# Kernel tuning notes

Hardware: AMD Instinct MI355X
Metric: run time of the kernel (lower is better)

The kernel has to match this reference:

```python
import jax, jax.numpy as jnp
import numpy as np

N_NODES = 100000
N_EDGES = 1600000
IN_DIM = 128
LATENT = [128, 128, 16]  # last entry = num classes (logits dim)


def setup_inputs() -> dict:
    key = jax.random.key(0)
    ks = jax.random.split(key, 16)
    inp = {
        "x": jax.random.normal(ks[0], (N_NODES, IN_DIM), dtype=jnp.float32),
        "edge_index": jax.random.randint(ks[1], (2, N_EDGES), 0, N_NODES, dtype=jnp.int64),
        "edge_weight": jax.random.uniform(ks[2], (N_EDGES,), dtype=jnp.float32),
    }
    dims = [IN_DIM] + LATENT
    for i in range(len(LATENT)):
        fan_in = dims[i]
        scale = 1.0 / np.sqrt(fan_in)
        inp[f"W{i}"] = jax.random.uniform(ks[3 + 2 * i], (dims[i], dims[i + 1]), minval=-scale, maxval=scale, dtype=jnp.float32)
        inp[f"b{i}"] = jax.random.uniform(ks[4 + 2 * i], (dims[i + 1],), minval=-scale, maxval=scale, dtype=jnp.float32)
        inp[f"eps{i}"] = jnp.zeros((), dtype=jnp.float32)  # GINConv train_eps init = 0
    return inp


def _gin_layer(x, W, b, eps, src, dst, edge_weight):
    # message: x_j (optionally scaled by edge weight), summed into target nodes
    msg = x[src]
    if edge_weight is not None:
        msg = msg * edge_weight[:, None]
    agg = jax.ops.segment_sum(msg, dst, num_segments=N_NODES)
    h = (1.0 + eps) * x + agg
    return jax.nn.relu(h @ W + b)  # MLP = Linear + ReLU


def _l2_normalize(x, eps=1e-12):
    norm = jnp.linalg.norm(x, axis=-1, keepdims=True)
    return x / jnp.maximum(norm, eps)


def reference(x, edge_index, edge_weight, W0, b0, eps0, W1, b1, eps1, W2, b2, eps2):
    src, dst = edge_index[0], edge_index[1]
    params = [(W0, b0, eps0), (W1, b1, eps1), (W2, b2, eps2)]
    h = x
    # all but last layer: GINConv(with edge_weight) -> l2 normalize -> ReLU
    for (W, b, e) in params[:-1]:
        h = _gin_layer(h, W, b, e, src, dst, edge_weight)
        h = _l2_normalize(h)  # emb_normlize=True
        h = jax.nn.relu(h)
    # last layer: GINConv WITHOUT edge_weight (forward passes only x, edge_index)
    W, b, e = params[-1]
    logits = _gin_layer(h, W, b, e, src, dst, None)
    probs = jax.nn.softmax(logits, axis=-1)
    return (logits, probs)
```

## Files before the change

kernel.cpp:

```cpp
#include <hip/hip_runtime.h>
#include <hip/hip_bf16.h>

#define N_NODES 100000
#define N_EDGES 1600000
#define DIM 128
#define ODIM 16
#define NB 391
#define PCHUNK 3200
#define PBLK 500
#define FCAP 4608
#define CB4 12500

typedef unsigned int uint32;
typedef float f32x2 __attribute__((ext_vector_type(2)));
typedef float f32x4 __attribute__((ext_vector_type(4)));
typedef short bf16x8 __attribute__((ext_vector_type(8)));
typedef uint32 u32x4 __attribute__((ext_vector_type(4)));
typedef uint32 u32x2 __attribute__((ext_vector_type(2)));

static __device__ __forceinline__ float bflo(uint32 p) { return __uint_as_float(p << 16); }
static __device__ __forceinline__ float bfhi(uint32 p) { return __uint_as_float(p & 0xFFFF0000u); }
static __device__ __forceinline__ unsigned short f2bf(float f) {
  __hip_bfloat16 h = __float2bfloat16(f);
  return *reinterpret_cast<unsigned short*>(&h);
}
static __device__ __forceinline__ uint32 pk2bf(float a, float b) {
  return (uint32)f2bf(a) | ((uint32)f2bf(b) << 16);
}

__global__ __launch_bounds__(256) void prep_kernel(
    const f32x4* __restrict__ x4, uint32* __restrict__ Xu,
    const float* __restrict__ W0, const float* __restrict__ W1,
    const float* __restrict__ W2,
    unsigned short* __restrict__ pW0, unsigned short* __restrict__ pW1,
    unsigned short* __restrict__ pW2,
    const int* __restrict__ dst, int* __restrict__ bcnt) {
  __shared__ int h[NB];
  int b = blockIdx.x;
  int tid = threadIdx.x;
  if (b < CB4) {
    int i = b * 256 + tid;
    f32x4 v = __builtin_nontemporal_load(x4 + i);
    u32x2 o = {pk2bf(v[0], v[1]), pk2bf(v[2], v[3])};
    *(u32x2*)(Xu + (size_t)i * 2) = o;
  } else if (b < CB4 + 128) {
    int wsel = (b - CB4) >> 6;
    int idx = ((b - CB4) & 63) * 256 + tid;
    int j = idx & 7, lane = (idx >> 3) & 63, nt = (idx >> 9) & 7, kc = idx >> 12;
    const float* W = wsel ? W1 : W0;
    unsigned short* pW = wsel ? pW1 : pW0;
    pW[idx] = f2bf(W[(kc * 32 + (lane >> 4) * 8 + j) * DIM + nt * 16 + (lane & 15)]);
  } else if (b < CB4 + 136) {
    int idx = (b - CB4 - 128) * 256 + tid;
    int j = idx & 7, lane = (idx >> 3) & 63, kc = idx >> 9;
    pW2[idx] = f2bf(W2[(kc * 32 + (lane >> 4) * 8 + j) * ODIM + (lane & 15)]);
  } else {
    for (int i = tid; i < NB; i += 256) h[i] = 0;
    __syncthreads();
    int e0 = (b - CB4 - 136) * PCHUNK;
    for (int i = tid; i < PCHUNK; i += 256)
      atomicAdd(&h[__builtin_nontemporal_load(dst + e0 + i) >> 8], 1);
    __syncthreads();
    for (int i = tid; i < NB; i += 256)
      if (h[i]) atomicAdd(&bcnt[i], h[i]);
  }
}

__global__ __launch_bounds__(256) void coarse_partition_kernel(
    const int* __restrict__ src, const int* __restrict__ dst,
    const float* __restrict__ ew, const int* __restrict__ bcnt,
    int* __restrict__ bcur, int2* __restrict__ epack) {
  __shared__ int hist[NB];
  __shared__ int base_a[NB];
  __shared__ int base_g[NB];
  __shared__ int lcur_a[NB];
  __shared__ int gbase_a[NB];
  __shared__ int2 stg[PCHUNK];
  __shared__ int gpos[PCHUNK];

  int tid = threadIdx.x;
  int e0 = blockIdx.x * PCHUNK;

  for (int i = tid; i < NB; i += 256) hist[i] = 0;
  __syncthreads();
  for (int i = tid; i < PCHUNK; i += 256) atomicAdd(&hist[dst[e0 + i] >> 8], 1);
  __syncthreads();

  if (tid < 64) {
    int run = 0, rung = 0;
#pragma unroll
    for (int c = 0; c < 7; c++) {
      int idx = c * 64 + tid;
      int v = (idx < NB) ? hist[idx] : 0;
      int vg = (idx < NB) ? bcnt[idx] : 0;
      int incl = v, inclg = vg;
#pragma unroll
      for (int off = 1; off < 64; off <<= 1) {
        int t1 = __shfl_up(incl, off, 64);
        int t2 = __shfl_up(inclg, off, 64);
        if (tid >= off) { incl += t1; inclg += t2; }
      }
      if (idx < NB) {
        base_a[idx] = run + incl - v;
        base_g[idx] = rung + inclg - vg;
      }
      run += __shfl(incl, 63, 64);
      rung += __shfl(inclg, 63, 64);
    }
  }
  __syncthreads();
  for (int i = tid; i < NB; i += 256) {
    int c = hist[i];
    gbase_a[i] = (c > 0) ? base_g[i] + atomicAdd(&bcur[i], c) : 0;
    lcur_a[i] = base_a[i];
  }
  __syncthreads();

  for (int i = tid; i < PCHUNK; i += 256) {
    int e = e0 + i;
    int s = __builtin_nontemporal_load(src + e);
    int d = dst[e];
    float w = __builtin_nontemporal_load(ew + e);
    int bkt = d >> 8;
    int pos = atomicAdd(&lcur_a[bkt], 1);
    stg[pos] = make_int2(s | ((d & 255) << 20), __float_as_int(w));
    gpos[pos] = gbase_a[bkt] + (pos - base_a[bkt]);
  }
  __syncthreads();
  for (int i = tid; i < PCHUNK; i += 256) epack[gpos[i]] = stg[i];
}

__global__ __launch_bounds__(256) void fine_sort_kernel(
    const int* __restrict__ bcnt, int2* __restrict__ epack,
    int* __restrict__ row_ptr) {
  __shared__ int2 ebuf[FCAP];
  __shared__ unsigned short inv[FCAP];
  __shared__ int hist[256];
  __shared__ int sc[256];
  __shared__ int cur[256];
  __shared__ int redc[4];
  int tid = threadIdx.x;
  int b = blockIdx.x;
  int node0 = b << 8;

  int part = 0;
  for (int i = tid; i < b; i += 256) part += bcnt[i];
#pragma unroll
  for (int off = 32; off >= 1; off >>= 1) part += __shfl_xor(part, off, 64);
  if ((tid & 63) == 0) redc[tid >> 6] = part;
  hist[tid] = 0;
  __syncthreads();
  int lo = redc[0] + redc[1] + redc[2] + redc[3];
  int n = bcnt[b];
  if (n > FCAP) n = FCAP;

  for (int i = tid; i < n; i += 256) {
    int2 e = epack[lo + i];
    ebuf[i] = e;
    atomicAdd(&hist[(e.x >> 20) & 255], 1);
  }
  __syncthreads();
  sc[tid] = hist[tid];
  __syncthreads();
  for (int off = 1; off < 256; off <<= 1) {
    int a2 = (tid >= off) ? sc[tid - off] : 0;
    __syncthreads();
    sc[tid] += a2;
    __syncthreads();
  }
  int excl = sc[tid] - hist[tid];
  if (node0 + tid < N_NODES) row_ptr[node0 + tid] = lo + excl;
  cur[tid] = excl;
  if (b == 0 && tid == 0) row_ptr[N_NODES] = N_EDGES;
  __syncthreads();
  for (int i = tid; i < n; i += 256) {
    int p = atomicAdd(&cur[(ebuf[i].x >> 20) & 255], 1);
    inv[p] = (unsigned short)i;
  }
  __syncthreads();
  for (int p = tid; p < n; p += 256) {
    int2 e = ebuf[inv[p]];
    epack[lo + p] = make_int2(e.x & 0xFFFFF, e.y);
  }
}

__global__ __launch_bounds__(256, 8) void gather_bf16(
    const uint32* __restrict__ hu, const int* __restrict__ row_ptr,
    const int2* __restrict__ ep, uint32* __restrict__ aggu) {
  int lane = threadIdx.x & 63;
  int node = blockIdx.x * 4 + (threadIdx.x >> 6);
  if (node >= N_NODES) return;
  int grp = lane >> 4, l4 = lane & 15;
  int a = row_ptr[node], bnd = row_ptr[node + 1];
  f32x2 acc2[4];
#pragma unroll
  for (int k = 0; k < 4; k++) acc2[k] = (f32x2){0.f, 0.f};

  auto acc8 = [&](float wv, const uint4& p) {
    acc2[0] += (f32x2){bflo(p.x), bfhi(p.x)} * wv;
    acc2[1] += (f32x2){bflo(p.y), bfhi(p.y)} * wv;
    acc2[2] += (f32x2){bflo(p.z), bfhi(p.z)} * wv;
    acc2[3] += (f32x2){bflo(p.w), bfhi(p.w)} * wv;
  };

#pragma unroll 2
  for (int j = a; j < bnd; j += 16) {
    int i0 = j + grp;
    int i1 = i0 + 4;
    int i2 = i0 + 8;
    int i3 = i0 + 12;
    int2 e0 = ep[i0 < bnd ? i0 : a];
    int2 e1 = ep[i1 < bnd ? i1 : a];
    int2 e2 = ep[i2 < bnd ? i2 : a];
    int2 e3 = ep[i3 < bnd ? i3 : a];
    uint4 p0 = *(const uint4*)(hu + (size_t)e0.x * 64 + l4 * 4);
    uint4 p1 = *(const uint4*)(hu + (size_t)e1.x * 64 + l4 * 4);
    uint4 p2 = *(const uint4*)(hu + (size_t)e2.x * 64 + l4 * 4);
    uint4 p3 = *(const uint4*)(hu + (size_t)e3.x * 64 + l4 * 4);
    float w0 = i0 < bnd ? __int_as_float(e0.y) : 0.f;
    float w1 = i1 < bnd ? __int_as_float(e1.y) : 0.f;
    float w2 = i2 < bnd ? __int_as_float(e2.y) : 0.f;
    float w3 = i3 < bnd ? __int_as_float(e3.y) : 0.f;
    acc8(w0, p0);
    acc8(w1, p1);
    acc8(w2, p2);
    acc8(w3, p3);
  }
#pragma unroll
  for (int k = 0; k < 4; k++) {
    acc2[k].x += __shfl_xor(acc2[k].x, 16, 64);
    acc2[k].x += __shfl_xor(acc2[k].x, 32, 64);
    acc2[k].y += __shfl_xor(acc2[k].y, 16, 64);
    acc2[k].y += __shfl_xor(acc2[k].y, 32, 64);
  }
  if (lane < 16) {
    u32x4 st = {pk2bf(acc2[0].x, acc2[0].y), pk2bf(acc2[1].x, acc2[1].y),
                pk2bf(acc2[2].x, acc2[2].y), pk2bf(acc2[3].x, acc2[3].y)};
    __builtin_nontemporal_store(st, (u32x4*)(aggu + (size_t)node * 64 + l4 * 4));
  }
}

template <int FUSE_PROJ>
__global__ __launch_bounds__(256) void gin_mlp_mfma(
    const uint32* Xu, const uint32* __restrict__ Au,
    const unsigned char* __restrict__ pW, const float* __restrict__ b,
    const float* __restrict__ eps_p, uint32* outH,
    const unsigned char* __restrict__ pW2, uint32* __restrict__ yb) {
  __shared__ __align__(16) unsigned char As[64 * 272];
  int tid = threadIdx.x;
  int node0 = blockIdx.x * 64;
  float epf = 1.0f + *eps_p;

  const uint4* X4 = (const uint4*)Xu;
  const uint4* A4 = (const uint4*)Au;
#pragma unroll
  for (int c = 0; c < 4; c++) {
    int t = c * 256 + tid;
    int n = t >> 4, s = t & 15;
    int node = node0 + n;
    int cn = node < N_NODES ? node : N_NODES - 1;
    uint4 xv = X4[(size_t)cn * 16 + s];
    uint4 av = A4[(size_t)cn * 16 + s];
    uint4 o;
    o.x = pk2bf(fmaf(epf, bflo(xv.x), bflo(av.x)), fmaf(epf, bfhi(xv.x), bfhi(av.x)));
    o.y = pk2bf(fmaf(epf, bflo(xv.y), bflo(av.y)), fmaf(epf, bfhi(xv.y), bfhi(av.y)));
    o.z = pk2bf(fmaf(epf, bflo(xv.z), bflo(av.z)), fmaf(epf, bfhi(xv.z), bfhi(av.z)));
    o.w = pk2bf(fmaf(epf, bflo(xv.w), bflo(av.w)), fmaf(epf, bfhi(xv.w), bfhi(av.w)));
    *(uint4*)(As + n * 272 + s * 16) = o;
  }
  __syncthreads();

  int w = tid >> 6, l = tid & 63;
  int m = l & 15, q = l >> 4;

  f32x4 acc[8];
#pragma unroll
  for (int nt = 0; nt < 8; nt++) acc[nt] = (f32x4){0.f, 0.f, 0.f, 0.f};

  const unsigned char* Abase = As + (w * 16 + m) * 272 + q * 16;
#pragma unroll
  for (int kc = 0; kc < 4; kc++) {
    bf16x8 af = *(const bf16x8*)(Abase + kc * 64);
#pragma unroll
    for (int nt = 0; nt < 8; nt++) {
      bf16x8 bfr = *(const bf16x8*)(pW + (size_t)((kc * 8 + nt) * 64 + l) * 16);
      acc[nt] = __builtin_amdgcn_mfma_f32_16x16x32_bf16(af, bfr, acc[nt], 0, 0, 0);
    }
  }

  float ss[4] = {0.f, 0.f, 0.f, 0.f};
#pragma unroll
  for (int nt = 0; nt < 8; nt++) {
    float bj = b[nt * 16 + m];
#pragma unroll
    for (int r = 0; r < 4; r++) {
      float v = fmaxf(acc[nt][r] + bj, 0.0f);
      acc[nt][r] = v;
      ss[r] += v * v;
    }
  }
#pragma unroll
  for (int r = 0; r < 4; r++) {
    float s = ss[r];
    s += __shfl_xor(s, 1, 64);
    s += __shfl_xor(s, 2, 64);
    s += __shfl_xor(s, 4, 64);
    s += __shfl_xor(s, 8, 64);
    ss[r] = 1.0f / fmaxf(sqrtf(s), 1e-12f);
  }
#pragma unroll
  for (int nt = 0; nt < 8; nt++) {
#pragma unroll
    for (int r = 0; r < 4; r++) {
      unsigned short hv = f2bf(acc[nt][r] * ss[r]);
      *(unsigned short*)(As + (w * 16 + q * 4 + r) * 272 + (nt * 16 + m) * 2) = hv;
    }
  }

  if (FUSE_PROJ) {
    f32x4 accy = (f32x4){0.f, 0.f, 0.f, 0.f};
#pragma unroll
    for (int kc = 0; kc < 4; kc++) {
      bf16x8 af = *(const bf16x8*)(Abase + kc * 64);
      bf16x8 bfr = *(const bf16x8*)(pW2 + (size_t)(kc * 64 + l) * 16);
      accy = __builtin_amdgcn_mfma_f32_16x16x32_bf16(af, bfr, accy, 0, 0, 0);
    }
#pragma unroll
    for (int r = 0; r < 4; r++) {
      float v = accy[r];
      float o = __shfl_xor(v, 1, 64);
      if (!(m & 1)) {
        int orow = node0 + w * 16 + q * 4 + r;
        if (orow < N_NODES) yb[(size_t)orow * 8 + (m >> 1)] = pk2bf(v, o);
      }
    }
  } else {
    __syncthreads();
    int rem = N_NODES - node0; if (rem > 64) rem = 64;
    for (int i = tid; i < 1024; i += 256) {
      int row = i >> 4, seg = i & 15;
      if (row < rem) {
        uint4 vv = *(const uint4*)(As + row * 272 + seg * 16);
        *(uint4*)((unsigned char*)outH + (size_t)(node0 + row) * 256 + seg * 16) = vv;
      }
    }
  }
}

__global__ __launch_bounds__(256) void gather16_final_kernel(
    const uint32* __restrict__ yb, const int* __restrict__ row_ptr,
    const int2* __restrict__ ep, const float* __restrict__ bb,
    const float* __restrict__ eps_p, float* __restrict__ out_logits,
    float* __restrict__ out_probs) {
  int lane = threadIdx.x & 63;
  int node = blockIdx.x * 4 + (threadIdx.x >> 6);
  if (node >= N_NODES) return;
  int f2 = lane & 3;
  int eq = lane >> 2;
  int a = row_ptr[node], bnd = row_ptr[node + 1];
  f32x4 acc = (f32x4){0.f, 0.f, 0.f, 0.f};
  for (int j = a; j < bnd; j += 16) {
    int idx = j + eq;
    int vld = idx < bnd;
    int2 e = ep[vld ? idx : a];
    u32x2 p = *(const u32x2*)(yb + (size_t)e.x * 8 + f2 * 2);
    if (vld) {
      acc[0] += bflo(p[0]); acc[1] += bfhi(p[0]);
      acc[2] += bflo(p[1]); acc[3] += bfhi(p[1]);
    }
  }
#pragma unroll
  for (int k = 0; k < 4; k++) {
#pragma unroll
    for (int off = 4; off <= 32; off <<= 1)
      acc[k] += __shfl_xor(acc[k], off, 64);
  }
  if (eq == 0) {
    float epf = 1.0f + *eps_p;
    u32x2 ys = *(const u32x2*)(yb + (size_t)node * 8 + f2 * 2);
    f32x4 lg;
    lg[0] = fmaxf(fmaf(epf, bflo(ys[0]), acc[0]) + bb[f2 * 4 + 0], 0.f);
    lg[1] = fmaxf(fmaf(epf, bfhi(ys[0]), acc[1]) + bb[f2 * 4 + 1], 0.f);
    lg[2] = fmaxf(fmaf(epf, bflo(ys[1]), acc[2]) + bb[f2 * 4 + 2], 0.f);
    lg[3] = fmaxf(fmaf(epf, bfhi(ys[1]), acc[3]) + bb[f2 * 4 + 3], 0.f);
    float mx = fmaxf(fmaxf(lg[0], lg[1]), fmaxf(lg[2], lg[3]));
    mx = fmaxf(mx, __shfl_xor(mx, 1, 4));
    mx = fmaxf(mx, __shfl_xor(mx, 2, 4));
    f32x4 ex;
    float s = 0.f;
#pragma unroll
    for (int k = 0; k < 4; k++) { ex[k] = __expf(lg[k] - mx); s += ex[k]; }
    s += __shfl_xor(s, 1, 4);
    s += __shfl_xor(s, 2, 4);
    float invs = 1.0f / s;
    size_t base = (size_t)node * ODIM + f2 * 4;
    *(f32x4*)(out_logits + base) = lg;
    f32x4 pr = {ex[0] * invs, ex[1] * invs, ex[2] * invs, ex[3] * invs};
    *(f32x4*)(out_probs + base) = pr;
  }
}

extern "C" void kernel_launch(void* const* d_in, const int* in_sizes, int n_in,
                              void* d_out, int out_size, void* d_ws, size_t ws_size,
                              hipStream_t stream) {
  const float* x = (const float*)d_in[0];
  const int* ei = (const int*)d_in[1];
  const float* ew = (const float*)d_in[2];
  const float* W0 = (const float*)d_in[3];
  const float* b0 = (const float*)d_in[4];
  const float* e0 = (const float*)d_in[5];
  const float* W1 = (const float*)d_in[6];
  const float* b1 = (const float*)d_in[7];
  const float* e1 = (const float*)d_in[8];
  const float* W2 = (const float*)d_in[9];
  const float* b2 = (const float*)d_in[10];
  const float* e2 = (const float*)d_in[11];
  float* out = (float*)d_out;

  const int* srcp = ei;
  const int* dstp = ei + N_EDGES;

  char* ws = (char*)d_ws;
  size_t off = 0;
  uint32* Agg = (uint32*)(ws + off);  off += (size_t)N_NODES * DIM * 2;
  uint32* Xb  = (uint32*)(ws + off);  off += (size_t)N_NODES * DIM * 2;
  uint32* H   = (uint32*)(ws + off);  off += (size_t)N_NODES * DIM * 2;
  int2* epack = (int2*)(ws + off);    off += (size_t)N_EDGES * 8;
  uint32* yb  = (uint32*)(ws + off);  off += (size_t)N_NODES * 8 * 4;
  int* row_ptr = (int*)(ws + off);    off += (size_t)(N_NODES + 16) * 4;
  int* bcnt   = (int*)(ws + off);     off += 2048;
  int* bcur   = (int*)(ws + off);     off += 2048;
  unsigned short* pW0 = (unsigned short*)(ws + off); off += 32768;
  unsigned short* pW1 = (unsigned short*)(ws + off); off += 32768;
  unsigned short* pW2 = (unsigned short*)(ws + off); off += 4096;

  hipMemsetAsync(bcnt, 0, 4096, stream);
  prep_kernel<<<CB4 + 136 + PBLK, 256, 0, stream>>>(
      (const f32x4*)x, Xb, W0, W1, W2, pW0, pW1, pW2, dstp, bcnt);

  coarse_partition_kernel<<<PBLK, 256, 0, stream>>>(srcp, dstp, ew, bcnt, bcur, epack);
  fine_sort_kernel<<<NB, 256, 0, stream>>>(bcnt, epack, row_ptr);

  int ggrid = (N_NODES + 3) / 4;
  int mgrid = (N_NODES + 63) / 64;

  gather_bf16<<<ggrid, 256, 0, stream>>>(Xb, row_ptr, epack, Agg);
  gin_mlp_mfma<0><<<mgrid, 256, 0, stream>>>(Xb, Agg, (const unsigned char*)pW0,
                                             b0, e0, H, nullptr, nullptr);
  gather_bf16<<<ggrid, 256, 0, stream>>>(H, row_ptr, epack, Agg);
  gin_mlp_mfma<1><<<mgrid, 256, 0, stream>>>(H, Agg, (const unsigned char*)pW1,
                                             b1, e1, nullptr,
                                             (const unsigned char*)pW2, yb);
  gather16_final_kernel<<<ggrid, 256, 0, stream>>>(yb, row_ptr, epack, b2, e2,
                                                   out, out + (size_t)N_NODES * ODIM);
}
```

Measured before the change: 362.9 us.

## Fuse neighbor gather into GIN MLP kernel, dropping the aggregation buffer

Merges the separate bf16 edge-gather kernel into the MFMA MLP kernel. Each wave now aggregates the neighbours of its 16 nodes one node at a time and adds the (1+eps)*x term. The result goes straight into shared memory as the GEMM A tile. This removes the write and re-read of the 100k×128 aggregation buffer and one kernel launch per layer. In exchange, the gather runs with far fewer waves in flight and walks the nodes sequentially with a dependent load chain per node, so latency hiding may suffer.

```diff
diff --git a/kernel.cpp b/kernel.cpp
--- a/kernel.cpp
+++ b/kernel.cpp
@@ -184,65 +184,10 @@
   }
 }
 
-__global__ __launch_bounds__(256, 8) void gather_bf16(
+template <int FUSE_PROJ>
+__global__ __launch_bounds__(256) void gin_fused(
     const uint32* __restrict__ hu, const int* __restrict__ row_ptr,
-    const int2* __restrict__ ep, uint32* __restrict__ aggu) {
-  int lane = threadIdx.x & 63;
-  int node = blockIdx.x * 4 + (threadIdx.x >> 6);
-  if (node >= N_NODES) return;
-  int grp = lane >> 4, l4 = lane & 15;
-  int a = row_ptr[node], bnd = row_ptr[node + 1];
-  f32x2 acc2[4];
-#pragma unroll
-  for (int k = 0; k < 4; k++) acc2[k] = (f32x2){0.f, 0.f};
-
-  auto acc8 = [&](float wv, const uint4& p) {
-    acc2[0] += (f32x2){bflo(p.x), bfhi(p.x)} * wv;
-    acc2[1] += (f32x2){bflo(p.y), bfhi(p.y)} * wv;
-    acc2[2] += (f32x2){bflo(p.z), bfhi(p.z)} * wv;
-    acc2[3] += (f32x2){bflo(p.w), bfhi(p.w)} * wv;
-  };
-
-#pragma unroll 2
-  for (int j = a; j < bnd; j += 16) {
-    int i0 = j + grp;
-    int i1 = i0 + 4;
-    int i2 = i0 + 8;
-    int i3 = i0 + 12;
-    int2 e0 = ep[i0 < bnd ? i0 : a];
-    int2 e1 = ep[i1 < bnd ? i1 : a];
-    int2 e2 = ep[i2 < bnd ? i2 : a];
-    int2 e3 = ep[i3 < bnd ? i3 : a];
-    uint4 p0 = *(const uint4*)(hu + (size_t)e0.x * 64 + l4 * 4);
-    uint4 p1 = *(const uint4*)(hu + (size_t)e1.x * 64 + l4 * 4);
-    uint4 p2 = *(const uint4*)(hu + (size_t)e2.x * 64 + l4 * 4);
-    uint4 p3 = *(const uint4*)(hu + (size_t)e3.x * 64 + l4 * 4);
-    float w0 = i0 < bnd ? __int_as_float(e0.y) : 0.f;
-    float w1 = i1 < bnd ? __int_as_float(e1.y) : 0.f;
-    float w2 = i2 < bnd ? __int_as_float(e2.y) : 0.f;
-    float w3 = i3 < bnd ? __int_as_float(e3.y) : 0.f;
-    acc8(w0, p0);
-    acc8(w1, p1);
-    acc8(w2, p2);
-    acc8(w3, p3);
-  }
-#pragma unroll
-  for (int k = 0; k < 4; k++) {
-    acc2[k].x += __shfl_xor(acc2[k].x, 16, 64);
-    acc2[k].x += __shfl_xor(acc2[k].x, 32, 64);
-    acc2[k].y += __shfl_xor(acc2[k].y, 16, 64);
-    acc2[k].y += __shfl_xor(acc2[k].y, 32, 64);
-  }
-  if (lane < 16) {
-    u32x4 st = {pk2bf(acc2[0].x, acc2[0].y), pk2bf(acc2[1].x, acc2[1].y),
-                pk2bf(acc2[2].x, acc2[2].y), pk2bf(acc2[3].x, acc2[3].y)};
-    __builtin_nontemporal_store(st, (u32x4*)(aggu + (size_t)node * 64 + l4 * 4));
-  }
-}
-
-template <int FUSE_PROJ>
-__global__ __launch_bounds__(256) void gin_mlp_mfma(
-    const uint32* Xu, const uint32* __restrict__ Au,
+    const int2* __restrict__ ep,
     const unsigned char* __restrict__ pW, const float* __restrict__ b,
     const float* __restrict__ eps_p, uint32* outH,
     const unsigned char* __restrict__ pW2, uint32* __restrict__ yb) {
@@ -251,39 +196,83 @@
   int node0 = blockIdx.x * 64;
   float epf = 1.0f + *eps_p;
 
-  const uint4* X4 = (const uint4*)Xu;
-  const uint4* A4 = (const uint4*)Au;
-#pragma unroll
-  for (int c = 0; c < 4; c++) {
-    int t = c * 256 + tid;
-    int n = t >> 4, s = t & 15;
+  int wv = tid >> 6, lane = tid & 63;
+  int grp = lane >> 4, l4 = lane & 15;
+  const uint4* X4 = (const uint4*)hu;
+
+#pragma unroll 1
+  for (int nn = 0; nn < 16; nn++) {
+    int n = wv * 16 + nn;
     int node = node0 + n;
-    int cn = node < N_NODES ? node : N_NODES - 1;
-    uint4 xv = X4[(size_t)cn * 16 + s];
-    uint4 av = A4[(size_t)cn * 16 + s];
-    uint4 o;
-    o.x = pk2bf(fmaf(epf, bflo(xv.x), bflo(av.x)), fmaf(epf, bfhi(xv.x), bfhi(av.x)));
-    o.y = pk2bf(fmaf(epf, bflo(xv.y), bflo(av.y)), fmaf(epf, bfhi(xv.y), bfhi(av.y)));
-    o.z = pk2bf(fmaf(epf, bflo(xv.z), bflo(av.z)), fmaf(epf, bfhi(xv.z), bfhi(av.z)));
-    o.w = pk2bf(fmaf(epf, bflo(xv.w), bflo(av.w)), fmaf(epf, bfhi(xv.w), bfhi(av.w)));
-    *(uint4*)(As + n * 272 + s * 16) = o;
-  }
-  __syncthreads();
-
-  int w = tid >> 6, l = tid & 63;
-  int m = l & 15, q = l >> 4;
+    int a = 0, bnd = 0;
+    if (node < N_NODES) { a = row_ptr[node]; bnd = row_ptr[node + 1]; }
+    f32x2 acc2[4];
+#pragma unroll
+    for (int k = 0; k < 4; k++) acc2[k] = (f32x2){0.f, 0.f};
+
+    auto acc8 = [&](float wvv, const uint4& p) {
+      acc2[0] += (f32x2){bflo(p.x), bfhi(p.x)} * wvv;
+      acc2[1] += (f32x2){bflo(p.y), bfhi(p.y)} * wvv;
+      acc2[2] += (f32x2){bflo(p.z), bfhi(p.z)} * wvv;
+      acc2[3] += (f32x2){bflo(p.w), bfhi(p.w)} * wvv;
+    };
+
+#pragma unroll 2
+    for (int j = a; j < bnd; j += 16) {
+      int i0 = j + grp;
+      int i1 = i0 + 4;
+      int i2 = i0 + 8;
+      int i3 = i0 + 12;
+      int2 e0 = ep[i0 < bnd ? i0 : a];
+      int2 e1 = ep[i1 < bnd ? i1 : a];
+      int2 e2 = ep[i2 < bnd ? i2 : a];
+      int2 e3 = ep[i3 < bnd ? i3 : a];
+      uint4 p0 = *(const uint4*)(hu + (size_t)e0.x * 64 + l4 * 4);
+      uint4 p1 = *(const uint4*)(hu + (size_t)e1.x * 64 + l4 * 4);
+      uint4 p2 = *(const uint4*)(hu + (size_t)e2.x * 64 + l4 * 4);
+      uint4 p3 = *(const uint4*)(hu + (size_t)e3.x * 64 + l4 * 4);
+      float w0 = i0 < bnd ? __int_as_float(e0.y) : 0.f;
+      float w1 = i1 < bnd ? __int_as_float(e1.y) : 0.f;
+      float w2 = i2 < bnd ? __int_as_float(e2.y) : 0.f;
+      float w3 = i3 < bnd ? __int_as_float(e3.y) : 0.f;
+      acc8(w0, p0);
+      acc8(w1, p1);
+      acc8(w2, p2);
+      acc8(w3, p3);
+    }
+#pragma unroll
+    for (int k = 0; k < 4; k++) {
+      acc2[k].x += __shfl_xor(acc2[k].x, 16, 64);
+      acc2[k].x += __shfl_xor(acc2[k].x, 32, 64);
+      acc2[k].y += __shfl_xor(acc2[k].y, 16, 64);
+      acc2[k].y += __shfl_xor(acc2[k].y, 32, 64);
+    }
+    if (lane < 16) {
+      int cn = node < N_NODES ? node : N_NODES - 1;
+      uint4 xv = X4[(size_t)cn * 16 + l4];
+      uint4 o;
+      o.x = pk2bf(fmaf(epf, bflo(xv.x), acc2[0].x), fmaf(epf, bfhi(xv.x), acc2[0].y));
+      o.y = pk2bf(fmaf(epf, bflo(xv.y), acc2[1].x), fmaf(epf, bfhi(xv.y), acc2[1].y));
+      o.z = pk2bf(fmaf(epf, bflo(xv.z), acc2[2].x), fmaf(epf, bfhi(xv.z), acc2[2].y));
+      o.w = pk2bf(fmaf(epf, bflo(xv.w), acc2[3].x), fmaf(epf, bfhi(xv.w), acc2[3].y));
+      *(uint4*)(As + n * 272 + l4 * 16) = o;
+    }
+  }
+  __syncthreads();
+
+  int m = lane & 15, q = lane >> 4;
 
   f32x4 acc[8];
 #pragma unroll
   for (int nt = 0; nt < 8; nt++) acc[nt] = (f32x4){0.f, 0.f, 0.f, 0.f};
 
-  const unsigned char* Abase = As + (w * 16 + m) * 272 + q * 16;
+  const unsigned char* Abase = As + (wv * 16 + m) * 272 + q * 16;
 #pragma unroll
   for (int kc = 0; kc < 4; kc++) {
     bf16x8 af = *(const bf16x8*)(Abase + kc * 64);
 #pragma unroll
     for (int nt = 0; nt < 8; nt++) {
-      bf16x8 bfr = *(const bf16x8*)(pW + (size_t)((kc * 8 + nt) * 64 + l) * 16);
+      bf16x8 bfr = *(const bf16x8*)(pW + (size_t)((kc * 8 + nt) * 64 + lane) * 16);
       acc[nt] = __builtin_amdgcn_mfma_f32_16x16x32_bf16(af, bfr, acc[nt], 0, 0, 0);
     }
   }
@@ -313,7 +302,7 @@
 #pragma unroll
     for (int r = 0; r < 4; r++) {
       unsigned short hv = f2bf(acc[nt][r] * ss[r]);
-      *(unsigned short*)(As + (w * 16 + q * 4 + r) * 272 + (nt * 16 + m) * 2) = hv;
+      *(unsigned short*)(As + (wv * 16 + q * 4 + r) * 272 + (nt * 16 + m) * 2) = hv;
     }
   }
 
@@ -322,7 +311,7 @@
 #pragma unroll
     for (int kc = 0; kc < 4; kc++) {
       bf16x8 af = *(const bf16x8*)(Abase + kc * 64);
-      bf16x8 bfr = *(const bf16x8*)(pW2 + (size_t)(kc * 64 + l) * 16);
+      bf16x8 bfr = *(const bf16x8*)(pW2 + (size_t)(kc * 64 + lane) * 16);
       accy = __builtin_amdgcn_mfma_f32_16x16x32_bf16(af, bfr, accy, 0, 0, 0);
     }
 #pragma unroll
@@ -330,7 +319,7 @@
       float v = accy[r];
       float o = __shfl_xor(v, 1, 64);
       if (!(m & 1)) {
-        int orow = node0 + w * 16 + q * 4 + r;
+        int orow = node0 + wv * 16 + q * 4 + r;
         if (orow < N_NODES) yb[(size_t)orow * 8 + (m >> 1)] = pk2bf(v, o);
       }
     }
@@ -422,7 +411,6 @@
 
   char* ws = (char*)d_ws;
   size_t off = 0;
-  uint32* Agg = (uint32*)(ws + off);  off += (size_t)N_NODES * DIM * 2;
   uint32* Xb  = (uint32*)(ws + off);  off += (size_t)N_NODES * DIM * 2;
   uint32* H   = (uint32*)(ws + off);  off += (size_t)N_NODES * DIM * 2;
   int2* epack = (int2*)(ws + off);    off += (size_t)N_EDGES * 8;
@@ -441,16 +429,15 @@
   coarse_partition_kernel<<<PBLK, 256, 0, stream>>>(srcp, dstp, ew, bcnt, bcur, epack);
   fine_sort_kernel<<<NB, 256, 0, stream>>>(bcnt, epack, row_ptr);
 
+  int mgrid = (N_NODES + 63) / 64;
   int ggrid = (N_NODES + 3) / 4;
-  int mgrid = (N_NODES + 63) / 64;
-
-  gather_bf16<<<ggrid, 256, 0, stream>>>(Xb, row_ptr, epack, Agg);
-  gin_mlp_mfma<0><<<mgrid, 256, 0, stream>>>(Xb, Agg, (const unsigned char*)pW0,
-                                             b0, e0, H, nullptr, nullptr);
-  gather_bf16<<<ggrid, 256, 0, stream>>>(H, row_ptr, epack, Agg);
-  gin_mlp_mfma<1><<<mgrid, 256, 0, stream>>>(H, Agg, (const unsigned char*)pW1,
-                                             b1, e1, nullptr,
-                                             (const unsigned char*)pW2, yb);
+
+  gin_fused<0><<<mgrid, 256, 0, stream>>>(Xb, row_ptr, epack,
+                                          (const unsigned char*)pW0, b0, e0,
+                                          H, nullptr, nullptr);
+  gin_fused<1><<<mgrid, 256, 0, stream>>>(H, row_ptr, epack,
+                                          (const unsigned char*)pW1, b1, e1,
+                                          nullptr, (const unsigned char*)pW2, yb);
   gather16_final_kernel<<<ggrid, 256, 0, stream>>>(yb, row_ptr, epack, b2, e2,
                                                    out, out + (size_t)N_NODES * ODIM);
 }
```

Result: slower. 429.2 us (+18.3%).

## Fuse self-term combine into gather and widen partition/sort kernels to 512 threads

Applied to the files above, without the earlier changes.

The gather kernel now reads the node's own features and writes (1+eps)*x + agg directly, so the MLP kernel loads a single combined tensor instead of both X and the aggregate. This removes one 25.6 MB read per layer from the MLP stage in exchange for a small extra read in the gather epilogue. Separately, the coarse partition and fine sort kernels move to 512-thread blocks, and the fine sort's 256-entry prefix scan is replaced by a single-wavefront shuffle scan to cut barrier rounds. Larger blocks use more registers per block and can lower occupancy. Shared-memory usage is unchanged.

```diff
diff --git a/kernel.cpp b/kernel.cpp
--- a/kernel.cpp
+++ b/kernel.cpp
@@ -66,7 +66,7 @@
   }
 }
 
-__global__ __launch_bounds__(256) void coarse_partition_kernel(
+__global__ __launch_bounds__(512) void coarse_partition_kernel(
     const int* __restrict__ src, const int* __restrict__ dst,
     const float* __restrict__ ew, const int* __restrict__ bcnt,
     int* __restrict__ bcur, int2* __restrict__ epack) {
@@ -81,9 +81,9 @@
   int tid = threadIdx.x;
   int e0 = blockIdx.x * PCHUNK;
 
-  for (int i = tid; i < NB; i += 256) hist[i] = 0;
-  __syncthreads();
-  for (int i = tid; i < PCHUNK; i += 256) atomicAdd(&hist[dst[e0 + i] >> 8], 1);
+  for (int i = tid; i < NB; i += 512) hist[i] = 0;
+  __syncthreads();
+  for (int i = tid; i < PCHUNK; i += 512) atomicAdd(&hist[dst[e0 + i] >> 8], 1);
   __syncthreads();
 
   if (tid < 64) {
@@ -109,14 +109,14 @@
     }
   }
   __syncthreads();
-  for (int i = tid; i < NB; i += 256) {
+  for (int i = tid; i < NB; i += 512) {
     int c = hist[i];
     gbase_a[i] = (c > 0) ? base_g[i] + atomicAdd(&bcur[i], c) : 0;
     lcur_a[i] = base_a[i];
   }
   __syncthreads();
 
-  for (int i = tid; i < PCHUNK; i += 256) {
+  for (int i = tid; i < PCHUNK; i += 512) {
     int e = e0 + i;
     int s = __builtin_nontemporal_load(src + e);
     int d = dst[e];
@@ -127,10 +127,10 @@
     gpos[pos] = gbase_a[bkt] + (pos - base_a[bkt]);
   }
   __syncthreads();
-  for (int i = tid; i < PCHUNK; i += 256) epack[gpos[i]] = stg[i];
-}
-
-__global__ __launch_bounds__(256) void fine_sort_kernel(
+  for (int i = tid; i < PCHUNK; i += 512) epack[gpos[i]] = stg[i];
+}
+
+__global__ __launch_bounds__(512) void fine_sort_kernel(
     const int* __restrict__ bcnt, int2* __restrict__ epack,
     int* __restrict__ row_ptr) {
   __shared__ int2 ebuf[FCAP];
@@ -138,47 +138,59 @@
   __shared__ int hist[256];
   __shared__ int sc[256];
   __shared__ int cur[256];
-  __shared__ int redc[4];
+  __shared__ int redc[8];
   int tid = threadIdx.x;
   int b = blockIdx.x;
   int node0 = b << 8;
 
   int part = 0;
-  for (int i = tid; i < b; i += 256) part += bcnt[i];
+  for (int i = tid; i < b; i += 512) part += bcnt[i];
 #pragma unroll
   for (int off = 32; off >= 1; off >>= 1) part += __shfl_xor(part, off, 64);
   if ((tid & 63) == 0) redc[tid >> 6] = part;
-  hist[tid] = 0;
-  __syncthreads();
-  int lo = redc[0] + redc[1] + redc[2] + redc[3];
+  if (tid < 256) hist[tid] = 0;
+  __syncthreads();
+  int lo = redc[0] + redc[1] + redc[2] + redc[3] +
+           redc[4] + redc[5] + redc[6] + redc[7];
   int n = bcnt[b];
   if (n > FCAP) n = FCAP;
 
-  for (int i = tid; i < n; i += 256) {
+  for (int i = tid; i < n; i += 512) {
     int2 e = epack[lo + i];
     ebuf[i] = e;
     atomicAdd(&hist[(e.x >> 20) & 255], 1);
   }
   __syncthreads();
-  sc[tid] = hist[tid];
-  __syncthreads();
-  for (int off = 1; off < 256; off <<= 1) {
-    int a2 = (tid >= off) ? sc[tid - off] : 0;
-    __syncthreads();
-    sc[tid] += a2;
-    __syncthreads();
-  }
-  int excl = sc[tid] - hist[tid];
-  if (node0 + tid < N_NODES) row_ptr[node0 + tid] = lo + excl;
-  cur[tid] = excl;
+  if (tid < 64) {
+    int run = 0;
+#pragma unroll
+    for (int c = 0; c < 4; c++) {
+      int idx = c * 64 + tid;
+      int v = hist[idx];
+      int incl = v;
+#pragma unroll
+      for (int off = 1; off < 64; off <<= 1) {
+        int tv = __shfl_up(incl, off, 64);
+        if (tid >= off) incl += tv;
+      }
+      sc[idx] = run + incl;
+      run += __shfl(incl, 63, 64);
+    }
+  }
+  __syncthreads();
+  if (tid < 256) {
+    int excl = sc[tid] - hist[tid];
+    if (node0 + tid < N_NODES) row_ptr[node0 + tid] = lo + excl;
+    cur[tid] = excl;
+  }
   if (b == 0 && tid == 0) row_ptr[N_NODES] = N_EDGES;
   __syncthreads();
-  for (int i = tid; i < n; i += 256) {
+  for (int i = tid; i < n; i += 512) {
     int p = atomicAdd(&cur[(ebuf[i].x >> 20) & 255], 1);
     inv[p] = (unsigned short)i;
   }
   __syncthreads();
-  for (int p = tid; p < n; p += 256) {
+  for (int p = tid; p < n; p += 512) {
     int2 e = ebuf[inv[p]];
     epack[lo + p] = make_int2(e.x & 0xFFFFF, e.y);
   }
@@ -186,7 +198,8 @@
 
 __global__ __launch_bounds__(256, 8) void gather_bf16(
     const uint32* __restrict__ hu, const int* __restrict__ row_ptr,
-    const int2* __restrict__ ep, uint32* __restrict__ aggu) {
+    const int2* __restrict__ ep, const float* __restrict__ eps_p,
+    uint32* __restrict__ cg) {
   int lane = threadIdx.x & 63;
   int node = blockIdx.x * 4 + (threadIdx.x >> 6);
   if (node >= N_NODES) return;
@@ -234,39 +247,35 @@
     acc2[k].y += __shfl_xor(acc2[k].y, 32, 64);
   }
   if (lane < 16) {
-    u32x4 st = {pk2bf(acc2[0].x, acc2[0].y), pk2bf(acc2[1].x, acc2[1].y),
-                pk2bf(acc2[2].x, acc2[2].y), pk2bf(acc2[3].x, acc2[3].y)};
-    __builtin_nontemporal_store(st, (u32x4*)(aggu + (size_t)node * 64 + l4 * 4));
+    float epf = 1.0f + *eps_p;
+    uint4 xv = *(const uint4*)(hu + (size_t)node * 64 + l4 * 4);
+    u32x4 st;
+    st[0] = pk2bf(fmaf(epf, bflo(xv.x), acc2[0].x), fmaf(epf, bfhi(xv.x), acc2[0].y));
+    st[1] = pk2bf(fmaf(epf, bflo(xv.y), acc2[1].x), fmaf(epf, bfhi(xv.y), acc2[1].y));
+    st[2] = pk2bf(fmaf(epf, bflo(xv.z), acc2[2].x), fmaf(epf, bfhi(xv.z), acc2[2].y));
+    st[3] = pk2bf(fmaf(epf, bflo(xv.w), acc2[3].x), fmaf(epf, bfhi(xv.w), acc2[3].y));
+    __builtin_nontemporal_store(st, (u32x4*)(cg + (size_t)node * 64 + l4 * 4));
   }
 }
 
 template <int FUSE_PROJ>
 __global__ __launch_bounds__(256) void gin_mlp_mfma(
-    const uint32* Xu, const uint32* __restrict__ Au,
+    const uint32* __restrict__ Cu,
     const unsigned char* __restrict__ pW, const float* __restrict__ b,
-    const float* __restrict__ eps_p, uint32* outH,
-    const unsigned char* __restrict__ pW2, uint32* __restrict__ yb) {
+    uint32* outH, const unsigned char* __restrict__ pW2,
+    uint32* __restrict__ yb) {
   __shared__ __align__(16) unsigned char As[64 * 272];
   int tid = threadIdx.x;
   int node0 = blockIdx.x * 64;
-  float epf = 1.0f + *eps_p;
-
-  const uint4* X4 = (const uint4*)Xu;
-  const uint4* A4 = (const uint4*)Au;
+
+  const uint4* C4 = (const uint4*)Cu;
 #pragma unroll
   for (int c = 0; c < 4; c++) {
     int t = c * 256 + tid;
     int n = t >> 4, s = t & 15;
     int node = node0 + n;
     int cn = node < N_NODES ? node : N_NODES - 1;
-    uint4 xv = X4[(size_t)cn * 16 + s];
-    uint4 av = A4[(size_t)cn * 16 + s];
-    uint4 o;
-    o.x = pk2bf(fmaf(epf, bflo(xv.x), bflo(av.x)), fmaf(epf, bfhi(xv.x), bfhi(av.x)));
-    o.y = pk2bf(fmaf(epf, bflo(xv.y), bflo(av.y)), fmaf(epf, bfhi(xv.y), bfhi(av.y)));
-    o.z = pk2bf(fmaf(epf, bflo(xv.z), bflo(av.z)), fmaf(epf, bfhi(xv.z), bfhi(av.z)));
-    o.w = pk2bf(fmaf(epf, bflo(xv.w), bflo(av.w)), fmaf(epf, bfhi(xv.w), bfhi(av.w)));
-    *(uint4*)(As + n * 272 + s * 16) = o;
+    *(uint4*)(As + n * 272 + s * 16) = C4[(size_t)cn * 16 + s];
   }
   __syncthreads();
 
@@ -422,7 +431,7 @@
 
   char* ws = (char*)d_ws;
   size_t off = 0;
-  uint32* Agg = (uint32*)(ws + off);  off += (size_t)N_NODES * DIM * 2;
+  uint32* Cg  = (uint32*)(ws + off);  off += (size_t)N_NODES * DIM * 2;
   uint32* Xb  = (uint32*)(ws + off);  off += (size_t)N_NODES * DIM * 2;
   uint32* H   = (uint32*)(ws + off);  off += (size_t)N_NODES * DIM * 2;
   int2* epack = (int2*)(ws + off);    off += (size_t)N_EDGES * 8;
@@ -438,19 +447,18 @@
   prep_kernel<<<CB4 + 136 + PBLK, 256, 0, stream>>>(
       (const f32x4*)x, Xb, W0, W1, W2, pW0, pW1, pW2, dstp, bcnt);
 
-  coarse_partition_kernel<<<PBLK, 256, 0, stream>>>(srcp, dstp, ew, bcnt, bcur, epack);
-  fine_sort_kernel<<<NB, 256, 0, stream>>>(bcnt, epack, row_ptr);
+  coarse_partition_kernel<<<PBLK, 512, 0, stream>>>(srcp, dstp, ew, bcnt, bcur, epack);
+  fine_sort_kernel<<<NB, 512, 0, stream>>>(bcnt, epack, row_ptr);
 
   int ggrid = (N_NODES + 3) / 4;
   int mgrid = (N_NODES + 63) / 64;
 
-  gather_bf16<<<ggrid, 256, 0, stream>>>(Xb, row_ptr, epack, Agg);
-  gin_mlp_mfma<0><<<mgrid, 256, 0, stream>>>(Xb, Agg, (const unsigned char*)pW0,
-                                             b0, e0, H, nullptr, nullptr);
-  gather_bf16<<<ggrid, 256, 0, stream>>>(H, row_ptr, epack, Agg);
-  gin_mlp_mfma<1><<<mgrid, 256, 0, stream>>>(H, Agg, (const unsigned char*)pW1,
-                                             b1, e1, nullptr,
-                                             (const unsigned char*)pW2, yb);
+  gather_bf16<<<ggrid, 256, 0, stream>>>(Xb, row_ptr, epack, e0, Cg);
+  gin_mlp_mfma<0><<<mgrid, 256, 0, stream>>>(Cg, (const unsigned char*)pW0, b0,
+                                             H, nullptr, nullptr);
+  gather_bf16<<<ggrid, 256, 0, stream>>>(H, row_ptr, epack, e1, Cg);
+  gin_mlp_mfma<1><<<mgrid, 256, 0, stream>>>(Cg, (const unsigned char*)pW1, b1,
+                                             nullptr, (const unsigned char*)pW2, yb);
   gather16_final_kernel<<<ggrid, 256, 0, stream>>>(yb, row_ptr, epack, b2, e2,
                                                    out, out + (size_t)N_NODES * ODIM);
 }
```

After: 356.5 us. Within noise of the previous version (-1.8%).
